# Kernel optimization log

Measured on AMD Instinct MI355X. Metric: run time of the kernel, lower is better.

## Reference

```python
import jax, jax.numpy as jnp
import numpy as np

A_ANCHORS = 102400
BATCH = 16
N_ANN = 32
OMEGA = 3.0
EPSILON = 2.0
WING_C = OMEGA - OMEGA * float(np.log(1.0 + OMEGA / EPSILON))


def _calc_iou(a, b):
    # a: [A,4] anchors, b: [N,4] gt boxes -> [A,N]
    area = (b[:, 2] - b[:, 0]) * (b[:, 3] - b[:, 1])
    iw = jnp.minimum(a[:, 2][:, None], b[None, :, 2]) - jnp.maximum(a[:, 0][:, None], b[None, :, 0])
    ih = jnp.minimum(a[:, 3][:, None], b[None, :, 3]) - jnp.maximum(a[:, 1][:, None], b[None, :, 1])
    iw = jnp.clip(iw, 0.0)
    ih = jnp.clip(ih, 0.0)
    ua = ((a[:, 2] - a[:, 0]) * (a[:, 3] - a[:, 1]))[:, None] + area[None, :] - iw * ih
    ua = jnp.clip(ua, 1e-8)
    return iw * ih / ua


def setup_inputs() -> dict:
    rng = np.random.default_rng(0)
    B, N, A = BATCH, N_ANN, A_ANCHORS
    x1 = rng.uniform(1.0, 500.0, (B, N)).astype(np.float32)
    y1 = rng.uniform(1.0, 500.0, (B, N)).astype(np.float32)
    w = rng.uniform(16.0, 100.0, (B, N)).astype(np.float32)
    h = rng.uniform(16.0, 100.0, (B, N)).astype(np.float32)
    boxes = np.stack([x1, y1, x1 + w, y1 + h], axis=-1)
    # last 12 annotations per image are padding (first coord <= 0)
    boxes[:, 20:, 0] -= 600.0
    boxes[:, 20:, 2] -= 600.0
    ldm = rng.uniform(0.0, 640.0, (B, N, 196)).astype(np.float32)
    ldm[:, ::5, :] = 0.0  # some faces have no landmark annotation
    annotations = np.concatenate([boxes, ldm], axis=-1)
    ax1 = rng.uniform(0.0, 560.0, (A,)).astype(np.float32)
    ay1 = rng.uniform(0.0, 560.0, (A,)).astype(np.float32)
    aw = rng.uniform(16.0, 80.0, (A,)).astype(np.float32)
    ah = rng.uniform(16.0, 80.0, (A,)).astype(np.float32)
    anchor = np.stack([ax1, ay1, ax1 + aw, ay1 + ah], axis=-1)
    # plant jittered copies of valid GT boxes so IoU>=0.7 positives exist
    slot = 0
    for j in range(B):
        for k in range(20):
            for _ in range(4):
                anchor[slot] = boxes[j, k] + rng.uniform(-1.5, 1.5, (4,)).astype(np.float32)
                slot += 1
    anchors = anchor[None, :, :]
    k1, k2, k3 = jax.random.split(jax.random.key(0), 3)
    return {
        "classifications": jax.random.normal(k1, (B, A, 2), jnp.float32),
        "bbox_regressions": jax.random.normal(k2, (B, A, 4), jnp.float32),
        "ldm_regressions": jax.random.normal(k3, (B, A, 196), jnp.float32),
        "anchors": jnp.asarray(anchors),
        "annotations": jnp.asarray(annotations),
    }


def reference(classifications, bbox_regressions, ldm_regressions, anchors, annotations):
    anchor = anchors[0]
    A = anchor.shape[0]
    aw = anchor[:, 2] - anchor[:, 0]
    ah = anchor[:, 3] - anchor[:, 1]
    acx = anchor[:, 0] + 0.5 * aw
    acy = anchor[:, 1] + 0.5 * ah
    bbox_scale = jnp.array([0.1, 0.1, 0.2, 0.2], jnp.float32)
    even = (jnp.arange(196) % 2) == 0
    ctr = jnp.where(even, acx[:, None], acy[:, None])         # [A,196]
    den = jnp.where(even, aw[:, None], ah[:, None]) + 1e-14   # [A,196]
    s = jnp.concatenate([jnp.ones(68, jnp.float32), 3.0 * jnp.ones(128, jnp.float32)])
    arange_A = jnp.arange(A)

    def per_sample(cls, breg, lreg, ann):
        valid = ann[:, 0] > 0
        boxes = ann[:, :4]
        ldm_ann = ann[:, 4:]
        has_gt = jnp.any(valid)
        iou = _calc_iou(anchor, boxes)
        iou = jnp.where(valid[None, :], iou, -1.0)  # mask invalid GT
        iou_max = iou.max(axis=1)
        iou_arg = iou.argmax(axis=1)
        neg = iou_max < 0.4
        pos = iou_max >= 0.7
        npos = pos.sum()
        nneg = neg.sum()
        # hard-negative mining: keep top-(3*npos) negative scores
        keep = jnp.minimum(nneg, 3 * npos)
        neg_losses = jnp.where(neg, -cls[:, 1], -jnp.inf)
        sorted_neg = jnp.sort(neg_losses)[::-1]
        neg_mean = jnp.where(arange_A < keep, sorted_neg, 0.0).sum() / jnp.maximum(keep, 1)
        pos_mean = jnp.where(pos, -cls[:, 0], 0.0).sum() / jnp.maximum(npos, 1)
        cls_loss = jnp.where(has_gt & (npos > 0), pos_mean + neg_mean, 0.0)
        gb = boxes[iou_arg]
        gw = gb[:, 2] - gb[:, 0]
        gh = gb[:, 3] - gb[:, 1]
        gcx = gb[:, 0] + 0.5 * gw
        gcy = gb[:, 1] + 0.5 * gh
        tdx = (gcx - acx) / (aw + 1e-14)
        tdy = (gcy - acy) / (ah + 1e-14)
        tdw = jnp.log(gw / aw)
        tdh = jnp.log(gh / ah)
        btgt = jnp.stack([tdx, tdy, tdw, tdh], axis=1) / bbox_scale
        d = jnp.abs(btgt - breg)
        sl1 = jnp.where(d < 1.0, 0.5 * d * d, d - 0.5)
        bbox_loss = jnp.where(
            has_gt & (npos > 0),
            jnp.where(pos[:, None], sl1, 0.0).sum() / (jnp.maximum(npos, 1) * 4),
            0.0,
        )
        # landmark wing loss over positive anchors whose GT has landmarks
        gl = ldm_ann[iou_arg]  # [A,196]
        lpos = pos & (gl.sum(axis=1) > 0)
        nl = lpos.sum()
        ltgt = (gl - ctr) / den / 0.1
        dd = jnp.abs(ltgt * s - lreg * s)
        wing = jnp.where(dd < OMEGA, OMEGA * jnp.log1p(dd / EPSILON), dd - WING_C)
        ldm_loss = jnp.where(
            has_gt & (nl > 0),
            jnp.where(lpos[:, None], wing, 0.0).sum() / (jnp.maximum(nl, 1) * 196),
            0.0,
        )
        return cls_loss, bbox_loss, ldm_loss

    return jax.vmap(per_sample)(classifications, bbox_regressions, ldm_regressions, annotations)
```

## Files before the change

### kernel.cpp

```cpp
#include <hip/hip_runtime.h>

#define A_ANCH 102400
#define BATCH  16
#define N_ANN  32
#define NLDM   196
#define ANNW   200
#define BLOCKS_PER 400
#define NSLOT  32


#define OFF_ACC     0
#define OFF_NEGSUM  512
#define OFF_CANDCNT 4096
#define OFF_META    8192
#define OFF_PCNT    16384
#define OFF_HSLOT   131072
#define OFF_KEYS    (1u << 20)
#define OFF_CAND    (8u << 20)

__device__ __forceinline__ float key_to_val(unsigned kk) {
    unsigned vb = (kk & 0x80000000u) ? (kk ^ 0x80000000u) : ~kk;
    return __uint_as_float(vb);
}

__global__ __launch_bounds__(256) void k_zero(double* acc, double* negsum,
                                              int* cand_cnt, unsigned* histS) {
    int t = blockIdx.x * 256 + threadIdx.x;
    int nt = gridDim.x * 256;
    for (int i = t; i < BATCH * NSLOT * 256; i += nt) histS[i] = 0u;
    for (int i = t; i < BATCH * 3; i += nt) acc[i] = 0.0;
    for (int i = t; i < BATCH * 16; i += nt) negsum[i] = 0.0;
    for (int i = t; i < BATCH * 32; i += nt) cand_cnt[i] = 0;
}

__global__ __launch_bounds__(256) void k_main(
    const float* __restrict__ cls,
    const float* __restrict__ breg,
    const float* __restrict__ lreg,
    const float* __restrict__ anchors,
    const float* __restrict__ ann,
    double* __restrict__ acc,
    int4* __restrict__ pcnt,
    unsigned* __restrict__ keys,
    unsigned* __restrict__ histS)
{
    const int tid = threadIdx.x;
    const int b = blockIdx.x / BLOCKS_PER;
    const int blk = blockIdx.x % BLOCKS_PER;
    const int a = blk * 256 + tid;

    __shared__ float4 sbox[N_ANN];
    __shared__ int    svalid[N_ANN];
    __shared__ int    bh[256];
    __shared__ int    s_cnt[4][3];
    __shared__ double s_sum[4][3];
    bh[tid] = 0;
    if (tid < N_ANN) {
        float4 bx = *reinterpret_cast<const float4*>(ann + (size_t)(b * N_ANN + tid) * ANNW);
        sbox[tid] = bx;
        svalid[tid] = bx.x > 0.0f;
    }
    __syncthreads();

    float4 av = *reinterpret_cast<const float4*>(anchors + (size_t)a * 4);
    const float aw = av.z - av.x, ah = av.w - av.y;
    const float areaA = aw * ah;

    float best = -1e30f; int arg = 0;
    #pragma unroll
    for (int j = 0; j < N_ANN; ++j) {
        float4 bx = sbox[j];
        float areaB = (bx.z - bx.x) * (bx.w - bx.y);
        float iw = fminf(av.z, bx.z) - fmaxf(av.x, bx.x);
        float ih = fminf(av.w, bx.w) - fmaxf(av.y, bx.y);
        iw = fmaxf(iw, 0.0f); ih = fmaxf(ih, 0.0f);
        float inter = iw * ih;
        float ua = fmaxf(areaA + areaB - inter, 1e-8f);
        float v = svalid[j] ? (inter / ua) : -1.0f;
        if (v > best) { best = v; arg = j; }
    }
    const bool pos = best >= 0.7f;
    const bool neg = best < 0.4f;

    float2 c = *reinterpret_cast<const float2*>(cls + ((size_t)b * A_ANCH + a) * 2);

    float nv = -c.y;
    unsigned bits = __float_as_uint(nv);
    unsigned key = (bits & 0x80000000u) ? ~bits : (bits ^ 0x80000000u);
    keys[(size_t)b * A_ANCH + a] = neg ? key : 0u;
    if (neg) atomicAdd(&bh[key >> 24], 1);

    double v_pos = 0.0, v_bb = 0.0, v_ldm = 0.0;
    float glsum = 0.0f;
    const float acx = av.x + 0.5f * aw, acy = av.y + 0.5f * ah;

    if (pos) {
        v_pos = (double)(-c.x);

        float4 gb = sbox[arg];
        float gw = gb.z - gb.x, gh = gb.w - gb.y;
        float gcx = gb.x + 0.5f * gw, gcy = gb.y + 0.5f * gh;
        float t0 = ((gcx - acx) / (aw + 1e-14f)) / 0.1f;
        float t1 = ((gcy - acy) / (ah + 1e-14f)) / 0.1f;
        float t2 = logf(gw / aw) / 0.2f;
        float t3 = logf(gh / ah) / 0.2f;

        float4 rv = *reinterpret_cast<const float4*>(breg + ((size_t)b * A_ANCH + a) * 4);
        float bsum = 0.0f, d;
        d = fabsf(t0 - rv.x); bsum += (d < 1.0f) ? 0.5f * d * d : d - 0.5f;
        d = fabsf(t1 - rv.y); bsum += (d < 1.0f) ? 0.5f * d * d : d - 0.5f;
        d = fabsf(t2 - rv.z); bsum += (d < 1.0f) ? 0.5f * d * d : d - 0.5f;
        d = fabsf(t3 - rv.w); bsum += (d < 1.0f) ? 0.5f * d * d : d - 0.5f;
        v_bb = (double)bsum;

        const float* gl = ann + (size_t)(b * N_ANN + arg) * ANNW + 4;
        for (int i = 0; i < NLDM; i += 4) {
            float4 g4 = *reinterpret_cast<const float4*>(gl + i);
            glsum += g4.x + g4.y + g4.z + g4.w;
        }
    }
    const bool lpos = pos && (glsum > 0.0f);
    if (lpos) {
        const float* gl = ann + (size_t)(b * N_ANN + arg) * ANNW + 4;
        const float* lr = lreg + ((size_t)b * A_ANCH + a) * NLDM;
        const float inv_aw = 1.0f / ((aw + 1e-14f) * 0.1f);
        const float inv_ah = 1.0f / ((ah + 1e-14f) * 0.1f);
        double wsum = 0.0;
        for (int i = 0; i < NLDM; i += 4) {
            float4 l4 = *reinterpret_cast<const float4*>(lr + i);
            float4 g4 = *reinterpret_cast<const float4*>(gl + i);
            float s = (i < 68) ? 1.0f : 3.0f;
            float lt0 = (g4.x - acx) * inv_aw;
            float lt1 = (g4.y - acy) * inv_ah;
            float lt2 = (g4.z - acx) * inv_aw;
            float lt3 = (g4.w - acy) * inv_ah;
            float d0 = fabsf(lt0 * s - l4.x * s);
            float d1 = fabsf(lt1 * s - l4.y * s);
            float d2 = fabsf(lt2 * s - l4.z * s);
            float d3 = fabsf(lt3 * s - l4.w * s);
            float w0 = (d0 < 3.0f) ? 3.0f * log1pf(d0 * 0.5f) : d0 - 0.25112780437753474f;
            float w1 = (d1 < 3.0f) ? 3.0f * log1pf(d1 * 0.5f) : d1 - 0.25112780437753474f;
            float w2 = (d2 < 3.0f) ? 3.0f * log1pf(d2 * 0.5f) : d2 - 0.25112780437753474f;
            float w3 = (d3 < 3.0f) ? 3.0f * log1pf(d3 * 0.5f) : d3 - 0.25112780437753474f;
            wsum += (double)w0 + (double)w1 + (double)w2 + (double)w3;
        }
        v_ldm = wsum;
    }

    unsigned long long bp = __ballot(pos);
    unsigned long long bn = __ballot(neg);
    unsigned long long bl = __ballot(lpos);
    const int wave = tid >> 6, lane = tid & 63;
    if (lane == 0) {
        s_cnt[wave][0] = (int)__popcll(bp);
        s_cnt[wave][1] = (int)__popcll(bn);
        s_cnt[wave][2] = (int)__popcll(bl);
    }
    if (bp) {
        #pragma unroll
        for (int off = 32; off > 0; off >>= 1) {
            v_pos += __shfl_down(v_pos, off);
            v_bb  += __shfl_down(v_bb, off);
            v_ldm += __shfl_down(v_ldm, off);
        }
    }
    if (lane == 0) {
        s_sum[wave][0] = v_pos;
        s_sum[wave][1] = v_bb;
        s_sum[wave][2] = v_ldm;
    }
    __syncthreads();
    if (tid == 0) {
        int np = s_cnt[0][0] + s_cnt[1][0] + s_cnt[2][0] + s_cnt[3][0];
        int nn = s_cnt[0][1] + s_cnt[1][1] + s_cnt[2][1] + s_cnt[3][1];
        int nl = s_cnt[0][2] + s_cnt[1][2] + s_cnt[2][2] + s_cnt[3][2];
        pcnt[b * BLOCKS_PER + blk] = make_int4(np, nn, nl, 0);
        if (np > 0) {
            atomicAdd(&acc[b * 3 + 0], s_sum[0][0] + s_sum[1][0] + s_sum[2][0] + s_sum[3][0]);
            atomicAdd(&acc[b * 3 + 1], s_sum[0][1] + s_sum[1][1] + s_sum[2][1] + s_sum[3][1]);
            atomicAdd(&acc[b * 3 + 2], s_sum[0][2] + s_sum[1][2] + s_sum[2][2] + s_sum[3][2]);
        }
    }
    if (bh[tid]) {
        unsigned slot = (unsigned)(blockIdx.x & (NSLOT - 1));
        atomicAdd(&histS[((unsigned)b * NSLOT + slot) * 256u + (unsigned)tid],
                  (unsigned)bh[tid]);
    }
}

__global__ __launch_bounds__(256) void k_derive(
    const float* __restrict__ ann,
    const int4* __restrict__ pcnt,
    const unsigned* __restrict__ histS,
    int* __restrict__ meta)
{
    const int b = blockIdx.x;
    const int tid = threadIdx.x;

    __shared__ unsigned shist[256];
    __shared__ int s_c[4][3];
    __shared__ int s_hasgt;

    unsigned hsum = 0;
    #pragma unroll
    for (int s = 0; s < NSLOT; ++s)
        hsum += histS[((unsigned)b * NSLOT + s) * 256u + tid];
    shist[tid] = hsum;

    int np = 0, nn = 0, nl = 0;
    for (int i = tid; i < BLOCKS_PER; i += 256) {
        int4 p = pcnt[b * BLOCKS_PER + i];
        np += p.x; nn += p.y; nl += p.z;
    }
    #pragma unroll
    for (int off = 32; off > 0; off >>= 1) {
        np += __shfl_down(np, off);
        nn += __shfl_down(nn, off);
        nl += __shfl_down(nl, off);
    }
    const int wave = tid >> 6, lane = tid & 63;
    if (lane == 0) { s_c[wave][0] = np; s_c[wave][1] = nn; s_c[wave][2] = nl; }

    bool v = (tid < N_ANN) && (ann[(size_t)(b * N_ANN + tid) * ANNW] > 0.0f);
    unsigned long long bm = __ballot(v);
    if (tid == 0) s_hasgt = (bm != 0ull) ? 1 : 0;
    __syncthreads();

    if (tid == 0) {
        int tnp = s_c[0][0] + s_c[1][0] + s_c[2][0] + s_c[3][0];
        int tnn = s_c[0][1] + s_c[1][1] + s_c[2][1] + s_c[3][1];
        int tnl = s_c[0][2] + s_c[1][2] + s_c[2][2] + s_c[3][2];
        int keep = min(tnn, 3 * tnp);
        int bin0 = -1, rem = 0;
        if (keep > 0) {
            unsigned cum = 0;
            for (int i = 255; i >= 0; --i) {
                unsigned cc = shist[i];
                if (cum + cc >= (unsigned)keep) { bin0 = i; rem = keep - (int)cum; break; }
                cum += cc;
            }
        }
        meta[b * 8 + 0] = tnp;
        meta[b * 8 + 1] = tnn;
        meta[b * 8 + 2] = tnl;
        meta[b * 8 + 3] = keep;
        meta[b * 8 + 4] = bin0;
        meta[b * 8 + 5] = rem;
        meta[b * 8 + 6] = s_hasgt;
        meta[b * 8 + 7] = 0;
    }
}

__global__ __launch_bounds__(256) void k_pass1(
    const unsigned* __restrict__ keys,
    const int* __restrict__ meta,
    double* __restrict__ negsum,
    int* __restrict__ cand_cnt,
    unsigned* __restrict__ cand)
{
    const int tid = threadIdx.x;
    const int b = blockIdx.x >> 4;
    const int chunk = blockIdx.x & 15;
    const int CHUNK = A_ANCH / 16;

    const int keep = meta[b * 8 + 3];
    const int bin0i = meta[b * 8 + 4];
    if (keep <= 0 || bin0i < 0) return;
    const unsigned bin0 = (unsigned)bin0i;

    const unsigned* k = keys + (size_t)b * A_ANCH + (size_t)chunk * CHUNK;
    double lsum = 0.0;
    const int lane = tid & 63;
    for (int i = tid; i < CHUNK; i += 256) {
        unsigned kk = k[i];
        unsigned top = kk >> 24;
        if (top > bin0) lsum += (double)key_to_val(kk);
        bool match = (top == bin0);
        unsigned long long m = __ballot(match);
        if (m) {
            int leader = __ffsll((long long)m) - 1;
            int base = 0;
            if (lane == leader) base = atomicAdd(&cand_cnt[b * 32], (int)__popcll(m));
            base = __shfl(base, leader);
            if (match) {
                int rank = (int)__popcll(m & ((1ull << lane) - 1ull));
                cand[(size_t)b * A_ANCH + base + rank] = kk;
            }
        }
    }
    #pragma unroll
    for (int off = 32; off > 0; off >>= 1) lsum += __shfl_down(lsum, off);
    __shared__ double sred[4];
    if (lane == 0) sred[tid >> 6] = lsum;
    __syncthreads();
    if (tid == 0)
        negsum[b * 16 + chunk] = sred[0] + sred[1] + sred[2] + sred[3];
}

__global__ __launch_bounds__(256) void k_final(
    const double* __restrict__ acc,
    const int* __restrict__ meta,
    const double* __restrict__ negsum,
    const int* __restrict__ cand_cnt,
    const unsigned* __restrict__ cand,
    float* __restrict__ out)
{
    const int b = blockIdx.x;
    const int tid = threadIdx.x;

    __shared__ unsigned sh[256];
    __shared__ unsigned s_prefix;
    __shared__ int s_r;
    __shared__ double sred[4];

    const int npos  = meta[b * 8 + 0];
    const int nl    = meta[b * 8 + 2];
    const int keep  = meta[b * 8 + 3];
    const int bin0i = meta[b * 8 + 4];
    const int rem0  = meta[b * 8 + 5];
    const int hasgt = meta[b * 8 + 6];
    const int c = cand_cnt[b * 32];

    double total = 0.0;
    if (keep > 0 && bin0i >= 0) {
        unsigned prefix = ((unsigned)bin0i) << 24;
        int rem = rem0;
        const unsigned* cd = cand + (size_t)b * A_ANCH;

        for (int pass = 1; pass < 4; ++pass) {
            const int shift = 24 - 8 * pass;
            const unsigned maskAbove = 0xFFFFFFFFu << (shift + 8);
            __syncthreads();
            sh[tid] = 0;
            __syncthreads();
            for (int i = tid; i < c; i += 256) {
                unsigned kk = cd[i];
                if ((kk & maskAbove) == prefix)
                    atomicAdd(&sh[(kk >> shift) & 0xFFu], 1u);
            }
            __syncthreads();
            if (tid == 0) {
                unsigned cum = 0;
                for (int bin = 255; bin >= 0; --bin) {
                    unsigned cc = sh[bin];
                    if (cum + cc >= (unsigned)rem) {
                        s_r = rem - (int)cum;
                        s_prefix = prefix | ((unsigned)bin << shift);
                        break;
                    }
                    cum += cc;
                }
            }
            __syncthreads();
            prefix = s_prefix; rem = s_r;
        }
        const unsigned T = prefix;

        double lsum = 0.0;
        for (int i = tid; i < c; i += 256) {
            unsigned kk = cd[i];
            if (kk > T) lsum += (double)key_to_val(kk);
        }
        #pragma unroll
        for (int off = 32; off > 0; off >>= 1) lsum += __shfl_down(lsum, off);
        if ((tid & 63) == 0) sred[tid >> 6] = lsum;
        __syncthreads();
        if (tid == 0) {
            double ns = 0.0;
            for (int i = 0; i < 16; ++i) ns += negsum[b * 16 + i];
            total = ns + sred[0] + sred[1] + sred[2] + sred[3]
                  + (double)rem * (double)key_to_val(T);
        }
    }

    if (tid == 0) {
        double cls_l = 0.0, bbox_l = 0.0, ldm_l = 0.0;
        if (hasgt && npos > 0) {
            double neg_mean = (keep > 0) ? total / (double)keep : 0.0;
            cls_l = acc[b * 3 + 0] / (double)npos + neg_mean;
            bbox_l = acc[b * 3 + 1] / ((double)npos * 4.0);
        }
        if (hasgt && nl > 0) {
            ldm_l = acc[b * 3 + 2] / ((double)nl * 196.0);
        }
        out[b]             = (float)cls_l;
        out[BATCH + b]     = (float)bbox_l;
        out[2 * BATCH + b] = (float)ldm_l;
    }
}

extern "C" void kernel_launch(void* const* d_in, const int* in_sizes, int n_in,
                              void* d_out, int out_size, void* d_ws, size_t ws_size,
                              hipStream_t stream) {
    const float* cls     = (const float*)d_in[0];
    const float* breg    = (const float*)d_in[1];
    const float* lreg    = (const float*)d_in[2];
    const float* anchors = (const float*)d_in[3];
    const float* ann     = (const float*)d_in[4];

    char* ws = (char*)d_ws;
    double*   acc      = (double*)(ws + OFF_ACC);
    double*   negsum   = (double*)(ws + OFF_NEGSUM);
    int*      cand_cnt = (int*)(ws + OFF_CANDCNT);
    int*      meta     = (int*)(ws + OFF_META);
    int4*     pcnt     = (int4*)(ws + OFF_PCNT);
    unsigned* histS    = (unsigned*)(ws + OFF_HSLOT);
    unsigned* keys     = (unsigned*)(ws + OFF_KEYS);
    unsigned* cand     = (unsigned*)(ws + OFF_CAND);
    float*    out      = (float*)d_out;

    hipLaunchKernelGGL(k_zero, dim3(64), dim3(256), 0, stream,
                       acc, negsum, cand_cnt, histS);
    hipLaunchKernelGGL(k_main, dim3(BATCH * BLOCKS_PER), dim3(256), 0, stream,
                       cls, breg, lreg, anchors, ann, acc, pcnt, keys, histS);
    hipLaunchKernelGGL(k_derive, dim3(BATCH), dim3(256), 0, stream,
                       ann, pcnt, histS, meta);
    hipLaunchKernelGGL(k_pass1, dim3(BATCH * 16), dim3(256), 0, stream,
                       keys, meta, negsum, cand_cnt, cand);
    hipLaunchKernelGGL(k_final, dim3(BATCH), dim3(256), 0, stream,
                       acc, meta, negsum, cand_cnt, cand, out);
}
```

Baseline: 176.8 us.

## Fuse derive/pass1/final into one per-batch select kernel and drop atomics

Merges the three post-processing kernels into a single 1024-thread block per image, which scans keys, compacts candidates into LDS (spilling to global past capacity), and runs the radix refinement locally. k_main now writes per-block partial sums instead of double atomics, the zeroing kernel is replaced by a memset, and the IoU argmax uses a division-free cross-multiplied comparison with GT boxes read straight from global memory. This cuts launches and global round-trips. The cost is that the key scan now runs on only 16 blocks, so less of the GPU is used for it. The cross-multiplied comparison also drops the validity check, so padded boxes rely on getting zero intersection.

```diff
diff --git a/kernel.cpp b/kernel.cpp
--- a/kernel.cpp
+++ b/kernel.cpp
@@ -7,30 +7,18 @@
 #define ANNW   200
 #define BLOCKS_PER 400
 #define NSLOT  32
-
-
-#define OFF_ACC     0
-#define OFF_NEGSUM  512
-#define OFF_CANDCNT 4096
-#define OFF_META    8192
-#define OFF_PCNT    16384
-#define OFF_HSLOT   131072
-#define OFF_KEYS    (1u << 20)
-#define OFF_CAND    (8u << 20)
+#define SEL_T  1024
+#define CAP    14336
+
+#define OFF_PCNT   (16u << 10)
+#define OFF_PSUM   (131072u)
+#define OFF_HSLOT  (294912u)
+#define OFF_KEYS   (1u << 20)
+#define OFF_SPILL  (8u << 20)
 
 __device__ __forceinline__ float key_to_val(unsigned kk) {
     unsigned vb = (kk & 0x80000000u) ? (kk ^ 0x80000000u) : ~kk;
     return __uint_as_float(vb);
-}
-
-__global__ __launch_bounds__(256) void k_zero(double* acc, double* negsum,
-                                              int* cand_cnt, unsigned* histS) {
-    int t = blockIdx.x * 256 + threadIdx.x;
-    int nt = gridDim.x * 256;
-    for (int i = t; i < BATCH * NSLOT * 256; i += nt) histS[i] = 0u;
-    for (int i = t; i < BATCH * 3; i += nt) acc[i] = 0.0;
-    for (int i = t; i < BATCH * 16; i += nt) negsum[i] = 0.0;
-    for (int i = t; i < BATCH * 32; i += nt) cand_cnt[i] = 0;
 }
 
 __global__ __launch_bounds__(256) void k_main(
@@ -39,8 +27,8 @@
     const float* __restrict__ lreg,
     const float* __restrict__ anchors,
     const float* __restrict__ ann,
-    double* __restrict__ acc,
     int4* __restrict__ pcnt,
+    double* __restrict__ psum,
     unsigned* __restrict__ keys,
     unsigned* __restrict__ histS)
 {
@@ -49,38 +37,34 @@
     const int blk = blockIdx.x % BLOCKS_PER;
     const int a = blk * 256 + tid;
 
-    __shared__ float4 sbox[N_ANN];
-    __shared__ int    svalid[N_ANN];
     __shared__ int    bh[256];
     __shared__ int    s_cnt[4][3];
     __shared__ double s_sum[4][3];
     bh[tid] = 0;
-    if (tid < N_ANN) {
-        float4 bx = *reinterpret_cast<const float4*>(ann + (size_t)(b * N_ANN + tid) * ANNW);
-        sbox[tid] = bx;
-        svalid[tid] = bx.x > 0.0f;
-    }
     __syncthreads();
 
     float4 av = *reinterpret_cast<const float4*>(anchors + (size_t)a * 4);
     const float aw = av.z - av.x, ah = av.w - av.y;
     const float areaA = aw * ah;
 
-    float best = -1e30f; int arg = 0;
-    #pragma unroll
+    const float* __restrict__ annb = ann + (size_t)b * N_ANN * ANNW;
+    float bnum = -1e30f, bden = 1.0f; int arg = 0;
+    #pragma unroll 8
     for (int j = 0; j < N_ANN; ++j) {
-        float4 bx = sbox[j];
+        float4 bx = *reinterpret_cast<const float4*>(annb + (size_t)j * ANNW);
         float areaB = (bx.z - bx.x) * (bx.w - bx.y);
         float iw = fminf(av.z, bx.z) - fmaxf(av.x, bx.x);
         float ih = fminf(av.w, bx.w) - fmaxf(av.y, bx.y);
         iw = fmaxf(iw, 0.0f); ih = fmaxf(ih, 0.0f);
         float inter = iw * ih;
         float ua = fmaxf(areaA + areaB - inter, 1e-8f);
-        float v = svalid[j] ? (inter / ua) : -1.0f;
-        if (v > best) { best = v; arg = j; }
-    }
-    const bool pos = best >= 0.7f;
-    const bool neg = best < 0.4f;
+        bool upd = inter * bden > bnum * ua;
+        bnum = upd ? inter : bnum;
+        bden = upd ? ua : bden;
+        arg  = upd ? j : arg;
+    }
+    const bool pos = bnum >= 0.7f * bden;
+    const bool neg = bnum <  0.4f * bden;
 
     float2 c = *reinterpret_cast<const float2*>(cls + ((size_t)b * A_ANCH + a) * 2);
 
@@ -97,7 +81,7 @@
     if (pos) {
         v_pos = (double)(-c.x);
 
-        float4 gb = sbox[arg];
+        float4 gb = *reinterpret_cast<const float4*>(annb + (size_t)arg * ANNW);
         float gw = gb.z - gb.x, gh = gb.w - gb.y;
         float gcx = gb.x + 0.5f * gw, gcy = gb.y + 0.5f * gh;
         float t0 = ((gcx - acx) / (aw + 1e-14f)) / 0.1f;
@@ -113,7 +97,7 @@
         d = fabsf(t3 - rv.w); bsum += (d < 1.0f) ? 0.5f * d * d : d - 0.5f;
         v_bb = (double)bsum;
 
-        const float* gl = ann + (size_t)(b * N_ANN + arg) * ANNW + 4;
+        const float* gl = annb + (size_t)arg * ANNW + 4;
         for (int i = 0; i < NLDM; i += 4) {
             float4 g4 = *reinterpret_cast<const float4*>(gl + i);
             glsum += g4.x + g4.y + g4.z + g4.w;
@@ -121,7 +105,7 @@
     }
     const bool lpos = pos && (glsum > 0.0f);
     if (lpos) {
-        const float* gl = ann + (size_t)(b * N_ANN + arg) * ANNW + 4;
+        const float* gl = annb + (size_t)arg * ANNW + 4;
         const float* lr = lreg + ((size_t)b * A_ANCH + a) * NLDM;
         const float inv_aw = 1.0f / ((aw + 1e-14f) * 0.1f);
         const float inv_ah = 1.0f / ((ah + 1e-14f) * 0.1f);
@@ -175,11 +159,10 @@
         int nn = s_cnt[0][1] + s_cnt[1][1] + s_cnt[2][1] + s_cnt[3][1];
         int nl = s_cnt[0][2] + s_cnt[1][2] + s_cnt[2][2] + s_cnt[3][2];
         pcnt[b * BLOCKS_PER + blk] = make_int4(np, nn, nl, 0);
-        if (np > 0) {
-            atomicAdd(&acc[b * 3 + 0], s_sum[0][0] + s_sum[1][0] + s_sum[2][0] + s_sum[3][0]);
-            atomicAdd(&acc[b * 3 + 1], s_sum[0][1] + s_sum[1][1] + s_sum[2][1] + s_sum[3][1]);
-            atomicAdd(&acc[b * 3 + 2], s_sum[0][2] + s_sum[1][2] + s_sum[2][2] + s_sum[3][2]);
-        }
+        size_t pbase = (size_t)(b * BLOCKS_PER + blk) * 3;
+        psum[pbase + 0] = s_sum[0][0] + s_sum[1][0] + s_sum[2][0] + s_sum[3][0];
+        psum[pbase + 1] = s_sum[0][1] + s_sum[1][1] + s_sum[2][1] + s_sum[3][1];
+        psum[pbase + 2] = s_sum[0][2] + s_sum[1][2] + s_sum[2][2] + s_sum[3][2];
     }
     if (bh[tid]) {
         unsigned slot = (unsigned)(blockIdx.x & (NSLOT - 1));
@@ -188,48 +171,68 @@
     }
 }
 
-__global__ __launch_bounds__(256) void k_derive(
+__global__ __launch_bounds__(SEL_T) void k_sel(
     const float* __restrict__ ann,
     const int4* __restrict__ pcnt,
+    const double* __restrict__ psum,
     const unsigned* __restrict__ histS,
-    int* __restrict__ meta)
+    const unsigned* __restrict__ keys,
+    unsigned* __restrict__ spill,
+    float* __restrict__ out)
 {
     const int b = blockIdx.x;
     const int tid = threadIdx.x;
+    const int wave = tid >> 6, lane = tid & 63;
 
     __shared__ unsigned shist[256];
-    __shared__ int s_c[4][3];
-    __shared__ int s_hasgt;
-
-    unsigned hsum = 0;
-    #pragma unroll
-    for (int s = 0; s < NSLOT; ++s)
-        hsum += histS[((unsigned)b * NSLOT + s) * 256u + tid];
-    shist[tid] = hsum;
+    __shared__ unsigned s_cand[CAP];
+    __shared__ int    sredi[16][3];
+    __shared__ double sredd[16][3];
+    __shared__ int    s_i[8];
+    __shared__ double s_d[4];
+    __shared__ unsigned s_prefix;
+    __shared__ int s_r;
+    __shared__ int s_cc;
+
+    if (tid < 256) {
+        unsigned h = 0;
+        #pragma unroll
+        for (int s = 0; s < NSLOT; ++s)
+            h += histS[((unsigned)b * NSLOT + s) * 256u + (unsigned)tid];
+        shist[tid] = h;
+    }
 
     int np = 0, nn = 0, nl = 0;
-    for (int i = tid; i < BLOCKS_PER; i += 256) {
+    double a0 = 0.0, a1 = 0.0, a2 = 0.0;
+    for (int i = tid; i < BLOCKS_PER; i += SEL_T) {
         int4 p = pcnt[b * BLOCKS_PER + i];
         np += p.x; nn += p.y; nl += p.z;
+        size_t pbase = (size_t)(b * BLOCKS_PER + i) * 3;
+        a0 += psum[pbase + 0]; a1 += psum[pbase + 1]; a2 += psum[pbase + 2];
     }
     #pragma unroll
     for (int off = 32; off > 0; off >>= 1) {
-        np += __shfl_down(np, off);
-        nn += __shfl_down(nn, off);
-        nl += __shfl_down(nl, off);
-    }
-    const int wave = tid >> 6, lane = tid & 63;
-    if (lane == 0) { s_c[wave][0] = np; s_c[wave][1] = nn; s_c[wave][2] = nl; }
-
-    bool v = (tid < N_ANN) && (ann[(size_t)(b * N_ANN + tid) * ANNW] > 0.0f);
-    unsigned long long bm = __ballot(v);
-    if (tid == 0) s_hasgt = (bm != 0ull) ? 1 : 0;
+        np += __shfl_down(np, off); nn += __shfl_down(nn, off); nl += __shfl_down(nl, off);
+        a0 += __shfl_down(a0, off); a1 += __shfl_down(a1, off); a2 += __shfl_down(a2, off);
+    }
+    if (lane == 0) {
+        sredi[wave][0] = np; sredi[wave][1] = nn; sredi[wave][2] = nl;
+        sredd[wave][0] = a0; sredd[wave][1] = a1; sredd[wave][2] = a2;
+    }
+
+    if (tid < 64) {
+        bool v = (tid < N_ANN) && (ann[(size_t)(b * N_ANN + tid) * ANNW] > 0.0f);
+        unsigned long long bm = __ballot(v);
+        if (tid == 0) s_i[6] = (bm != 0ull) ? 1 : 0;
+    }
     __syncthreads();
 
     if (tid == 0) {
-        int tnp = s_c[0][0] + s_c[1][0] + s_c[2][0] + s_c[3][0];
-        int tnn = s_c[0][1] + s_c[1][1] + s_c[2][1] + s_c[3][1];
-        int tnl = s_c[0][2] + s_c[1][2] + s_c[2][2] + s_c[3][2];
+        int tnp = 0, tnn = 0, tnl = 0; double t0 = 0, t1 = 0, t2 = 0;
+        for (int w = 0; w < 16; ++w) {
+            tnp += sredi[w][0]; tnn += sredi[w][1]; tnl += sredi[w][2];
+            t0 += sredd[w][0]; t1 += sredd[w][1]; t2 += sredd[w][2];
+        }
         int keep = min(tnn, 3 * tnp);
         int bin0 = -1, rem = 0;
         if (keep > 0) {
@@ -240,148 +243,116 @@
                 cum += cc;
             }
         }
-        meta[b * 8 + 0] = tnp;
-        meta[b * 8 + 1] = tnn;
-        meta[b * 8 + 2] = tnl;
-        meta[b * 8 + 3] = keep;
-        meta[b * 8 + 4] = bin0;
-        meta[b * 8 + 5] = rem;
-        meta[b * 8 + 6] = s_hasgt;
-        meta[b * 8 + 7] = 0;
-    }
-}
-
-__global__ __launch_bounds__(256) void k_pass1(
-    const unsigned* __restrict__ keys,
-    const int* __restrict__ meta,
-    double* __restrict__ negsum,
-    int* __restrict__ cand_cnt,
-    unsigned* __restrict__ cand)
-{
-    const int tid = threadIdx.x;
-    const int b = blockIdx.x >> 4;
-    const int chunk = blockIdx.x & 15;
-    const int CHUNK = A_ANCH / 16;
-
-    const int keep = meta[b * 8 + 3];
-    const int bin0i = meta[b * 8 + 4];
-    if (keep <= 0 || bin0i < 0) return;
-    const unsigned bin0 = (unsigned)bin0i;
-
-    const unsigned* k = keys + (size_t)b * A_ANCH + (size_t)chunk * CHUNK;
-    double lsum = 0.0;
-    const int lane = tid & 63;
-    for (int i = tid; i < CHUNK; i += 256) {
-        unsigned kk = k[i];
-        unsigned top = kk >> 24;
-        if (top > bin0) lsum += (double)key_to_val(kk);
-        bool match = (top == bin0);
-        unsigned long long m = __ballot(match);
-        if (m) {
-            int leader = __ffsll((long long)m) - 1;
-            int base = 0;
-            if (lane == leader) base = atomicAdd(&cand_cnt[b * 32], (int)__popcll(m));
-            base = __shfl(base, leader);
-            if (match) {
-                int rank = (int)__popcll(m & ((1ull << lane) - 1ull));
-                cand[(size_t)b * A_ANCH + base + rank] = kk;
-            }
-        }
-    }
-    #pragma unroll
-    for (int off = 32; off > 0; off >>= 1) lsum += __shfl_down(lsum, off);
-    __shared__ double sred[4];
-    if (lane == 0) sred[tid >> 6] = lsum;
-    __syncthreads();
-    if (tid == 0)
-        negsum[b * 16 + chunk] = sred[0] + sred[1] + sred[2] + sred[3];
-}
-
-__global__ __launch_bounds__(256) void k_final(
-    const double* __restrict__ acc,
-    const int* __restrict__ meta,
-    const double* __restrict__ negsum,
-    const int* __restrict__ cand_cnt,
-    const unsigned* __restrict__ cand,
-    float* __restrict__ out)
-{
-    const int b = blockIdx.x;
-    const int tid = threadIdx.x;
-
-    __shared__ unsigned sh[256];
-    __shared__ unsigned s_prefix;
-    __shared__ int s_r;
-    __shared__ double sred[4];
-
-    const int npos  = meta[b * 8 + 0];
-    const int nl    = meta[b * 8 + 2];
-    const int keep  = meta[b * 8 + 3];
-    const int bin0i = meta[b * 8 + 4];
-    const int rem0  = meta[b * 8 + 5];
-    const int hasgt = meta[b * 8 + 6];
-    const int c = cand_cnt[b * 32];
-
-    double total = 0.0;
-    if (keep > 0 && bin0i >= 0) {
-        unsigned prefix = ((unsigned)bin0i) << 24;
-        int rem = rem0;
-        const unsigned* cd = cand + (size_t)b * A_ANCH;
-
-        for (int pass = 1; pass < 4; ++pass) {
-            const int shift = 24 - 8 * pass;
-            const unsigned maskAbove = 0xFFFFFFFFu << (shift + 8);
-            __syncthreads();
-            sh[tid] = 0;
-            __syncthreads();
-            for (int i = tid; i < c; i += 256) {
-                unsigned kk = cd[i];
-                if ((kk & maskAbove) == prefix)
-                    atomicAdd(&sh[(kk >> shift) & 0xFFu], 1u);
-            }
-            __syncthreads();
-            if (tid == 0) {
-                unsigned cum = 0;
-                for (int bin = 255; bin >= 0; --bin) {
-                    unsigned cc = sh[bin];
-                    if (cum + cc >= (unsigned)rem) {
-                        s_r = rem - (int)cum;
-                        s_prefix = prefix | ((unsigned)bin << shift);
-                        break;
+        s_i[0] = tnp; s_i[1] = tnn; s_i[2] = tnl;
+        s_i[3] = keep; s_i[4] = bin0; s_i[5] = rem;
+        s_d[0] = t0; s_d[1] = t1; s_d[2] = t2;
+        s_cc = 0;
+    }
+    __syncthreads();
+
+    const int keep = s_i[3];
+    const int bin0 = s_i[4];
+    unsigned* sp = spill + (size_t)b * A_ANCH;
+
+    double lneg = 0.0;
+    if (keep > 0) {
+        const uint4* k4 = reinterpret_cast<const uint4*>(keys + (size_t)b * A_ANCH);
+        const unsigned long long lmask = (1ull << lane) - 1ull;
+        for (int i = tid; i < A_ANCH / 4; i += SEL_T) {
+            uint4 kv = k4[i];
+            #pragma unroll
+            for (int e = 0; e < 4; ++e) {
+                unsigned kk = (e == 0) ? kv.x : (e == 1) ? kv.y : (e == 2) ? kv.z : kv.w;
+                int top = (int)(kk >> 24);
+                if (top > bin0) lneg += (double)key_to_val(kk);
+                bool m = (top == bin0);
+                unsigned long long bm = __ballot(m);
+                if (bm) {
+                    int ldr = __ffsll((long long)bm) - 1;
+                    int base = 0;
+                    if (lane == ldr) base = atomicAdd(&s_cc, (int)__popcll(bm));
+                    base = __shfl(base, ldr);
+                    if (m) {
+                        int idx = base + (int)__popcll(bm & lmask);
+                        if (idx < CAP) s_cand[idx] = kk;
+                        else sp[idx - CAP] = kk;
                     }
-                    cum += cc;
                 }
             }
-            __syncthreads();
-            prefix = s_prefix; rem = s_r;
-        }
-        const unsigned T = prefix;
-
-        double lsum = 0.0;
-        for (int i = tid; i < c; i += 256) {
-            unsigned kk = cd[i];
-            if (kk > T) lsum += (double)key_to_val(kk);
-        }
-        #pragma unroll
-        for (int off = 32; off > 0; off >>= 1) lsum += __shfl_down(lsum, off);
-        if ((tid & 63) == 0) sred[tid >> 6] = lsum;
+        }
+    }
+    #pragma unroll
+    for (int off = 32; off > 0; off >>= 1) lneg += __shfl_down(lneg, off);
+    __syncthreads();
+    if (lane == 0) sredd[wave][0] = lneg;
+    __syncthreads();
+    if (tid == 0) {
+        double t = 0.0;
+        for (int w = 0; w < 16; ++w) t += sredd[w][0];
+        s_d[3] = t;
+        s_i[7] = s_cc;
+    }
+    __syncthreads();
+    const int cnt = s_i[7];
+
+    unsigned prefix = ((unsigned)bin0) << 24;
+    for (int pass = 1; pass < 4; ++pass) {
+        const int shift = 24 - 8 * pass;
+        const unsigned maskAbove = 0xFFFFFFFFu << (shift + 8);
+        if (tid < 256) shist[tid] = 0;
+        __syncthreads();
+        for (int i = tid; i < cnt; i += SEL_T) {
+            unsigned kk = (i < CAP) ? s_cand[i] : sp[i - CAP];
+            if ((kk & maskAbove) == prefix)
+                atomicAdd(&shist[(kk >> shift) & 0xFFu], 1u);
+        }
         __syncthreads();
         if (tid == 0) {
-            double ns = 0.0;
-            for (int i = 0; i < 16; ++i) ns += negsum[b * 16 + i];
-            total = ns + sred[0] + sred[1] + sred[2] + sred[3]
-                  + (double)rem * (double)key_to_val(T);
-        }
-    }
+            int rem = (pass == 1) ? s_i[5] : s_r;
+            unsigned cum = 0;
+            unsigned npre = prefix;
+            int nrem = rem;
+            for (int bin = 255; bin >= 0; --bin) {
+                unsigned cc = shist[bin];
+                if (cum + cc >= (unsigned)rem) {
+                    nrem = rem - (int)cum;
+                    npre = prefix | ((unsigned)bin << shift);
+                    break;
+                }
+                cum += cc;
+            }
+            s_r = nrem; s_prefix = npre;
+        }
+        __syncthreads();
+        prefix = s_prefix;
+    }
+    const unsigned T = prefix;
+
+    double ls = 0.0;
+    for (int i = tid; i < cnt; i += SEL_T) {
+        unsigned kk = (i < CAP) ? s_cand[i] : sp[i - CAP];
+        if (kk > T) ls += (double)key_to_val(kk);
+    }
+    #pragma unroll
+    for (int off = 32; off > 0; off >>= 1) ls += __shfl_down(ls, off);
+    __syncthreads();
+    if (lane == 0) sredd[wave][0] = ls;
+    __syncthreads();
 
     if (tid == 0) {
+        double cs = 0.0;
+        for (int w = 0; w < 16; ++w) cs += sredd[w][0];
+        double total = s_d[3] + cs + (double)s_r * (double)key_to_val(T);
+
+        const int npos = s_i[0], nlc = s_i[2], hasgt = s_i[6];
         double cls_l = 0.0, bbox_l = 0.0, ldm_l = 0.0;
         if (hasgt && npos > 0) {
             double neg_mean = (keep > 0) ? total / (double)keep : 0.0;
-            cls_l = acc[b * 3 + 0] / (double)npos + neg_mean;
-            bbox_l = acc[b * 3 + 1] / ((double)npos * 4.0);
-        }
-        if (hasgt && nl > 0) {
-            ldm_l = acc[b * 3 + 2] / ((double)nl * 196.0);
+            cls_l = s_d[0] / (double)npos + neg_mean;
+            bbox_l = s_d[1] / ((double)npos * 4.0);
+        }
+        if (hasgt && nlc > 0) {
+            ldm_l = s_d[2] / ((double)nlc * 196.0);
         }
         out[b]             = (float)cls_l;
         out[BATCH + b]     = (float)bbox_l;
@@ -399,24 +370,16 @@
     const float* ann     = (const float*)d_in[4];
 
     char* ws = (char*)d_ws;
-    double*   acc      = (double*)(ws + OFF_ACC);
-    double*   negsum   = (double*)(ws + OFF_NEGSUM);
-    int*      cand_cnt = (int*)(ws + OFF_CANDCNT);
-    int*      meta     = (int*)(ws + OFF_META);
-    int4*     pcnt     = (int4*)(ws + OFF_PCNT);
-    unsigned* histS    = (unsigned*)(ws + OFF_HSLOT);
-    unsigned* keys     = (unsigned*)(ws + OFF_KEYS);
-    unsigned* cand     = (unsigned*)(ws + OFF_CAND);
-    float*    out      = (float*)d_out;
-
-    hipLaunchKernelGGL(k_zero, dim3(64), dim3(256), 0, stream,
-                       acc, negsum, cand_cnt, histS);
+    int4*     pcnt  = (int4*)(ws + OFF_PCNT);
+    double*   psum  = (double*)(ws + OFF_PSUM);
+    unsigned* histS = (unsigned*)(ws + OFF_HSLOT);
+    unsigned* keys  = (unsigned*)(ws + OFF_KEYS);
+    unsigned* spill = (unsigned*)(ws + OFF_SPILL);
+    float*    out   = (float*)d_out;
+
+    hipMemsetAsync(histS, 0, (size_t)BATCH * NSLOT * 256 * 4, stream);
     hipLaunchKernelGGL(k_main, dim3(BATCH * BLOCKS_PER), dim3(256), 0, stream,
-                       cls, breg, lreg, anchors, ann, acc, pcnt, keys, histS);
-    hipLaunchKernelGGL(k_derive, dim3(BATCH), dim3(256), 0, stream,
-                       ann, pcnt, histS, meta);
-    hipLaunchKernelGGL(k_pass1, dim3(BATCH * 16), dim3(256), 0, stream,
-                       keys, meta, negsum, cand_cnt, cand);
-    hipLaunchKernelGGL(k_final, dim3(BATCH), dim3(256), 0, stream,
-                       acc, meta, negsum, cand_cnt, cand, out);
+                       cls, breg, lreg, anchors, ann, pcnt, psum, keys, histS);
+    hipLaunchKernelGGL(k_sel, dim3(BATCH), dim3(SEL_T), 0, stream,
+                       ann, pcnt, psum, histS, keys, spill, out);
 }
```

After: 157.6 us. 1.12x faster.
